# Kernel optimization log

Measured on AMD Instinct MI355X. Metric: run time of the kernel, lower is better.

Reference implementation:

```python
import jax, jax.numpy as jnp
import numpy as np

N = 100000      # nodes
E = 1600000     # edges (avg degree 16)
IN_DIM = 128
OUT_DIM = 64


def setup_inputs() -> dict:
    key = jax.random.key(0)
    k0, k1, k2, k3, k4 = jax.random.split(key, 5)
    h = jax.random.normal(k0, (N, IN_DIM), dtype=jnp.float32)
    src = jax.random.randint(k1, (E,), 0, N)
    dst = jax.random.randint(k2, (E,), 0, N)
    W = jax.random.normal(k3, (OUT_DIM, IN_DIM), dtype=jnp.float32) * 0.05  # fc.weight
    a = jax.random.normal(k4, (2 * OUT_DIM,), dtype=jnp.float32) * 0.05     # attn_fc.weight (flattened)
    return {"h": h, "src": src, "dst": dst, "W": W, "a": a}


def reference(h, src, dst, W, a):
    # z = fc(h)
    z = h @ W.T                                   # [N, OUT_DIM]
    # attn_fc([z_src, z_dst]) == z_src @ a[:D] + z_dst @ a[D:]  (exact linear split)
    s_src = z @ a[:OUT_DIM]                       # [N]
    s_dst = z @ a[OUT_DIM:]                       # [N]
    e = jax.nn.leaky_relu(s_src[src] + s_dst[dst], negative_slope=0.01)  # [E]
    # segment softmax over incoming edges of each dst node
    m = jax.ops.segment_max(e, dst, num_segments=N)
    m = jnp.where(jnp.isfinite(m), m, 0.0)        # empty segments -> -inf; neutralize
    ee = jnp.exp(e - m[dst])                      # [E]
    denom = jax.ops.segment_sum(ee, dst, num_segments=N)
    alpha = ee / jnp.where(denom == 0, 1.0, denom)[dst]
    # scatter-weighted sum of source features
    h_out = jax.ops.segment_sum(alpha[:, None] * z[src], dst, num_segments=N)  # [N, OUT_DIM]
    # activation = F.elu; residual disabled (in_dim != out_dim * num_heads)
    return jax.nn.elu(h_out)
```

## Files before the change

kernel.cpp:

```cpp
#include <hip/hip_runtime.h>
#include <hip/hip_bf16.h>
#include <math.h>

typedef float floatx4 __attribute__((ext_vector_type(4)));
typedef short short8 __attribute__((ext_vector_type(8)));

#define IN_DIM 128
#define OUT_DIM 64
#define OWNER(d) (((d) >> 4) & 7)
#define CHUNK 2048
#define CAP 32
#define OVF_CAP 8192
#define WPAD 136
#define NB_SHIFT 8
#define CELL_CAP 24
#define CHUNK1 4096
#define SPILL_BIT (1 << 20)

__device__ __forceinline__ unsigned short bf16_rne(float f) {
    unsigned u = __float_as_uint(f);
    u += 0x7FFFu + ((u >> 16) & 1u);
    return (unsigned short)(u >> 16);
}
__device__ __forceinline__ float bf16_tof(unsigned short b) {
    return __uint_as_float(((unsigned)b) << 16);
}

__global__ __launch_bounds__(256) void k_gemm(
    const float* __restrict__ h, const float* __restrict__ W,
    const float* __restrict__ a, __hip_bfloat16* __restrict__ z,
    float* __restrict__ s_src, float* __restrict__ s_dst, int N)
{
    __shared__ __align__(16) unsigned short sWhi[64 * WPAD];
    __shared__ __align__(16) unsigned short sWlo[64 * WPAD];

    const int tid = threadIdx.x;
#pragma unroll
    for (int i = 0; i < 32; ++i) {
        int g = tid + 256 * i;
        float f = W[g];
        int row = g >> 7, k = g & 127;
        unsigned short hb = bf16_rne(f);
        sWhi[row * WPAD + k] = hb;
        sWlo[row * WPAD + k] = bf16_rne(f - bf16_tof(hb));
    }

    const int wave = tid >> 6;
    const int l = tid & 63;
    const int lr = l & 15;
    const int lk = l >> 4;
    const int n0w = blockIdx.x * 64 + wave * 16;

    const int arow = min(n0w + lr, N - 1);
    const float* hrow = h + (size_t)arow * IN_DIM;
    short8 ahi[4], alo[4];
#pragma unroll
    for (int ks = 0; ks < 4; ++ks) {
        int k0 = 32 * ks + 8 * lk;
        floatx4 f0 = *(const floatx4*)(hrow + k0);
        floatx4 f1 = *(const floatx4*)(hrow + k0 + 4);
        float fv[8] = {f0.x, f0.y, f0.z, f0.w, f1.x, f1.y, f1.z, f1.w};
#pragma unroll
        for (int j = 0; j < 8; ++j) {
            unsigned short hb = bf16_rne(fv[j]);
            ahi[ks][j] = (short)hb;
            alo[ks][j] = (short)bf16_rne(fv[j] - bf16_tof(hb));
        }
    }
    __syncthreads();

    float ps[4] = {0.f, 0.f, 0.f, 0.f};
    float pd[4] = {0.f, 0.f, 0.f, 0.f};
#pragma unroll
    for (int ct = 0; ct < 4; ++ct) {
        floatx4 acc = (floatx4){0.f, 0.f, 0.f, 0.f};
#pragma unroll
        for (int ks = 0; ks < 4; ++ks) {
            const int boff = (ct * 16 + lr) * WPAD + 32 * ks + 8 * lk;
            short8 bhi = *(const short8*)&sWhi[boff];
            short8 blo = *(const short8*)&sWlo[boff];
            acc = __builtin_amdgcn_mfma_f32_16x16x32_bf16(ahi[ks], bhi, acc, 0, 0, 0);
            acc = __builtin_amdgcn_mfma_f32_16x16x32_bf16(alo[ks], bhi, acc, 0, 0, 0);
            acc = __builtin_amdgcn_mfma_f32_16x16x32_bf16(ahi[ks], blo, acc, 0, 0, 0);
        }
        const float asv = a[ct * 16 + lr];
        const float adv = a[OUT_DIM + ct * 16 + lr];
#pragma unroll
        for (int r = 0; r < 4; ++r) {
            int n = n0w + lk * 4 + r;
            if (n < N)
                z[(size_t)n * OUT_DIM + ct * 16 + lr] = __float2bfloat16(acc[r]);
            ps[r] += acc[r] * asv;
            pd[r] += acc[r] * adv;
        }
    }
#pragma unroll
    for (int r = 0; r < 4; ++r) {
#pragma unroll
        for (int off = 1; off <= 8; off <<= 1) {
            ps[r] += __shfl_xor(ps[r], off);
            pd[r] += __shfl_xor(pd[r], off);
        }
        int n = n0w + lk * 4 + r;
        if (lr == 0 && n < N) {
            s_src[n] = ps[r];
            s_dst[n] = pd[r];
        }
    }
}

__global__ __launch_bounds__(256) void k_bin(
    const int* __restrict__ src, const int* __restrict__ dst,
    int* __restrict__ cursor, unsigned* __restrict__ bdata,
    int* __restrict__ bcnt, int* __restrict__ ovfcnt,
    int2* __restrict__ ovf, int E, int NB)
{
    __shared__ int cell[512];
    const int tid = threadIdx.x;
    for (int i = tid; i < NB; i += 256) cell[i] = 0;
    __syncthreads();

    const int c = blockIdx.x;
    const int e0 = c * CHUNK1;
    const size_t cbase = (size_t)c * NB * CELL_CAP;
#pragma unroll
    for (int i = 0; i < CHUNK1 / 256; ++i) {
        int e = e0 + i * 256 + tid;
        if (e < E) {
            int d = __builtin_nontemporal_load(&dst[e]);
            int s = __builtin_nontemporal_load(&src[e]);
            int b = d >> NB_SHIFT;
            int slot = atomicAdd(&cell[b], 1);
            if (slot < CELL_CAP) {
                bdata[cbase + (size_t)b * CELL_CAP + slot] =
                    ((unsigned)s << 8) | (unsigned)(d & 255);
            } else {
                atomicAdd(&cursor[d], SPILL_BIT);
                int op = atomicAdd(ovfcnt, 1);
                if (op < OVF_CAP) ovf[op] = make_int2(s, d);
            }
        }
    }
    __syncthreads();
    for (int b = tid; b < NB; b += 256) bcnt[c * NB + b] = cell[b];
}

__global__ __launch_bounds__(256) void k_fill(
    const unsigned* __restrict__ bdata, const int* __restrict__ bcnt,
    int* __restrict__ cursor, int* __restrict__ ssort,
    int* __restrict__ ovfcnt, int2* __restrict__ ovf,
    int nb1, int NB, int N)
{
    __shared__ int lcur[256];
    const int tid = threadIdx.x;
    lcur[tid] = 0;
    __syncthreads();

    const int b = blockIdx.x;
    const int n0 = b << NB_SHIFT;
    for (int c = tid; c < nb1; c += 256) {
        int cnt = min(bcnt[c * NB + b], CELL_CAP);
        size_t base = ((size_t)c * NB + b) * CELL_CAP;
        for (int j = 0; j < cnt; ++j) {
            unsigned v = bdata[base + j];
            int i = (int)(v & 255u);
            int s = (int)(v >> 8);
            int slot = atomicAdd(&lcur[i], 1);
            if (slot < CAP) {
                ssort[(n0 + i) * CAP + slot] = s;
            } else {
                int op = atomicAdd(ovfcnt, 1);
                if (op < OVF_CAP) ovf[op] = make_int2(s, n0 + i);
            }
        }
    }
    __syncthreads();
    int n = n0 + tid;
    if (n < N) {
        int v = lcur[tid];
        if (v) cursor[n] += v;
    }
}

__global__ __launch_bounds__(256) void k_scatter(
    const int* __restrict__ src, const int* __restrict__ dst,
    int* __restrict__ cursor, int* __restrict__ ssort,
    int* __restrict__ ovfcnt, int2* __restrict__ ovf, int E)
{
    const int x = blockIdx.x & 7;
    const int c = blockIdx.x >> 3;
    const int e0 = c * CHUNK;
#pragma unroll
    for (int i = 0; i < CHUNK / 256; ++i) {
        int e = e0 + i * 256 + threadIdx.x;
        if (e < E) {
            int d = __builtin_nontemporal_load(&dst[e]);
            if (OWNER(d) == x) {
                int s = __builtin_nontemporal_load(&src[e]);
                int pos = atomicAdd(&cursor[d], 1);
                if (pos < CAP) {
                    ssort[d * CAP + pos] = s;
                } else {
                    int op = atomicAdd(ovfcnt, 1);
                    if (op < OVF_CAP) ovf[op] = make_int2(s, d);
                }
            }
        }
    }
}

__global__ __launch_bounds__(256) void k_node(
    const int* __restrict__ cursor, const int* __restrict__ ssort,
    const float* __restrict__ s_src, const float* __restrict__ s_dst,
    const int* __restrict__ ovfcnt, const int2* __restrict__ ovf,
    const __hip_bfloat16* __restrict__ z, float* __restrict__ out, int N)
{
    const int lane = threadIdx.x & 63;
    const int wave = threadIdx.x >> 6;
    const int n = blockIdx.x * 4 + wave;
    if (n >= N) return;

    const int lg = lane >> 4;
    const int lc = lane & 15;

    const int raw = cursor[n];
    if (raw == 0) {
        if (lg == 0) {
            floatx4 zero = (floatx4){0.f, 0.f, 0.f, 0.f};
            __builtin_nontemporal_store(zero, (floatx4*)&out[(size_t)n * OUT_DIM + 4 * lc]);
        }
        return;
    }
    const int low = raw & 0xFFFFF;
    const int deg = min(low, CAP);
    const int base = n * CAP;
    const float sdn = s_dst[n];

    float sum = 0.f;
    int sv = 0;
    float ev = 0.f;
    {
        int kk = lane;
        if (kk < deg) {
            sv = __builtin_nontemporal_load(&ssort[base + kk]);
            float sc = s_src[sv] + sdn;
            sc = sc > 0.f ? sc : 0.01f * sc;
            ev = __expf(sc);
        }
        sum += ev;
    }

    floatx4 acc = (floatx4){0.f, 0.f, 0.f, 0.f};
    for (int j = 0; j < deg; j += 8) {
        int jj0 = j + lg, jj1 = j + 4 + lg;
        bool ok0 = jj0 < deg, ok1 = jj1 < deg;
        int s0 = __shfl(sv, ok0 ? jj0 : 0);
        int s1 = __shfl(sv, ok1 ? jj1 : 0);
        float w0 = __shfl(ev, ok0 ? jj0 : 0);
        float w1 = __shfl(ev, ok1 ? jj1 : 0);
        w0 = ok0 ? w0 : 0.f;
        w1 = ok1 ? w1 : 0.f;
        int sa0 = ok0 ? s0 : 0;
        int sa1 = ok1 ? s1 : 0;
        uint2 v0 = *(const uint2*)&z[(size_t)sa0 * OUT_DIM + 4 * lc];
        uint2 v1 = *(const uint2*)&z[(size_t)sa1 * OUT_DIM + 4 * lc];
        acc.x += w0 * __uint_as_float(v0.x << 16);
        acc.y += w0 * __uint_as_float(v0.x & 0xFFFF0000u);
        acc.z += w0 * __uint_as_float(v0.y << 16);
        acc.w += w0 * __uint_as_float(v0.y & 0xFFFF0000u);
        acc.x += w1 * __uint_as_float(v1.x << 16);
        acc.y += w1 * __uint_as_float(v1.x & 0xFFFF0000u);
        acc.z += w1 * __uint_as_float(v1.y << 16);
        acc.w += w1 * __uint_as_float(v1.y & 0xFFFF0000u);
    }
    acc.x += __shfl_xor(acc.x, 16); acc.y += __shfl_xor(acc.y, 16);
    acc.z += __shfl_xor(acc.z, 16); acc.w += __shfl_xor(acc.w, 16);
    acc.x += __shfl_xor(acc.x, 32); acc.y += __shfl_xor(acc.y, 32);
    acc.z += __shfl_xor(acc.z, 32); acc.w += __shfl_xor(acc.w, 32);

    if (raw > CAP) {
        int oc = min(*ovfcnt, OVF_CAP);
        for (int i = 0; i < oc; ++i) {
            int2 p = ovf[i];
            if (p.y == n) {
                float sc = s_src[p.x] + sdn;
                sc = sc > 0.f ? sc : 0.01f * sc;
                float e2 = __expf(sc);
                if (lane == 0) sum += e2;
                uint2 v = *(const uint2*)&z[(size_t)p.x * OUT_DIM + 4 * lc];
                acc.x += e2 * __uint_as_float(v.x << 16);
                acc.y += e2 * __uint_as_float(v.x & 0xFFFF0000u);
                acc.z += e2 * __uint_as_float(v.y << 16);
                acc.w += e2 * __uint_as_float(v.y & 0xFFFF0000u);
            }
        }
    }

#pragma unroll
    for (int off = 32; off >= 1; off >>= 1) sum += __shfl_xor(sum, off);

    if (lg == 0) {
        float inv = 1.f / sum;
        floatx4 o;
        o.x = acc.x * inv; o.y = acc.y * inv;
        o.z = acc.z * inv; o.w = acc.w * inv;
        o.x = o.x > 0.f ? o.x : expm1f(o.x);
        o.y = o.y > 0.f ? o.y : expm1f(o.y);
        o.z = o.z > 0.f ? o.z : expm1f(o.z);
        o.w = o.w > 0.f ? o.w : expm1f(o.w);
        __builtin_nontemporal_store(o, (floatx4*)&out[(size_t)n * OUT_DIM + 4 * lc]);
    }
}

extern "C" void kernel_launch(void* const* d_in, const int* in_sizes, int n_in,
                              void* d_out, int out_size, void* d_ws, size_t ws_size,
                              hipStream_t stream)
{
    (void)n_in; (void)out_size;

    const float* h  = (const float*)d_in[0];
    const int* src  = (const int*)d_in[1];
    const int* dst  = (const int*)d_in[2];
    const float* W  = (const float*)d_in[3];
    const float* a  = (const float*)d_in[4];
    const int N = in_sizes[0] / IN_DIM;
    const int E = in_sizes[1];
    float* out = (float*)d_out;

    const int NB  = (N + 255) >> NB_SHIFT;
    const int nb1 = (E + CHUNK1 - 1) / CHUNK1;

    auto rnd = [](size_t b) { return (b + 255) & ~(size_t)255; };
    const size_t meta_ints = (size_t)NB * 256 + 1 + (size_t)nb1 * NB;
    const size_t need_bucket =
        rnd((size_t)N * OUT_DIM * 2) + 2 * rnd((size_t)N * 4) +
        rnd(meta_ints * 4) + rnd((size_t)OVF_CAP * 8) +
        rnd((size_t)N * CAP * 4) + rnd((size_t)nb1 * NB * CELL_CAP * 4);
    const bool bucketed = (NB <= 512) && (need_bucket <= ws_size);

    char* wsp = (char*)d_ws;
    size_t off = 0;
    auto alloc = [&](size_t bytes) -> void* {
        void* p = wsp + off;
        off = (off + bytes + 255) & ~(size_t)255;
        return p;
    };
    __hip_bfloat16* z = (__hip_bfloat16*)alloc((size_t)N * OUT_DIM * 2);
    float* s_src = (float*)alloc((size_t)N * 4);
    float* s_dst = (float*)alloc((size_t)N * 4);

    const int nchunks = (E + CHUNK - 1) / CHUNK;
    k_gemm<<<(N + 63) / 64, 256, 0, stream>>>(h, W, a, z, s_src, s_dst, N);

    if (bucketed) {
        int* cursor = (int*)alloc(meta_ints * 4);
        int* ovfcnt = cursor + (size_t)NB * 256;
        int* bcnt   = ovfcnt + 1;
        int2* ovf   = (int2*)alloc((size_t)OVF_CAP * 8);
        int* ssort  = (int*)alloc((size_t)N * CAP * 4);
        unsigned* bdata = (unsigned*)alloc((size_t)nb1 * NB * CELL_CAP * 4);

        hipMemsetAsync(cursor, 0, meta_ints * 4, stream);
        k_bin<<<nb1, 256, 0, stream>>>(src, dst, cursor, bdata, bcnt,
                                       ovfcnt, ovf, E, NB);
        k_fill<<<NB, 256, 0, stream>>>(bdata, bcnt, cursor, ssort,
                                       ovfcnt, ovf, nb1, NB, N);
        k_node<<<(N + 3) / 4, 256, 0, stream>>>(cursor, ssort, s_src, s_dst,
                                                ovfcnt, ovf, z, out, N);
    } else {
        int* cursor = (int*)alloc((size_t)(N + 1) * 4);
        int* ovfcnt = cursor + N;
        int2* ovf   = (int2*)alloc((size_t)OVF_CAP * 8);
        int* ssort  = (int*)alloc((size_t)N * CAP * 4);

        hipMemsetAsync(cursor, 0, (size_t)(N + 1) * 4, stream);
        k_scatter<<<nchunks * 8, 256, 0, stream>>>(src, dst, cursor, ssort,
                                                   ovfcnt, ovf, E);
        k_node<<<(N + 3) / 4, 256, 0, stream>>>(cursor, ssort, s_src, s_dst,
                                                ovfcnt, ovf, z, out, N);
    }
}
```

Before: 213.6 us.

## Fuse bin and fill kernels with grid barrier, fold memset into GEMM

Merges the binning and fill kernels into one launch that uses a global atomic grid barrier between the two phases. The barrier relies on every block being resident at once (grid of max(NB, nb1) ≈ 391 blocks); if they were not, it would deadlock. The cursor/counter memset is moved into the GEMM kernel, so the separate hipMemsetAsync goes away. The ELU now uses __expf-1 instead of expm1f, which is cheaper but loses accuracy near zero. The aim is to remove launch and memset overhead.

Measured after the change: 267.6 us. 1.25x slower.

```diff
diff --git a/kernel.cpp b/kernel.cpp
--- a/kernel.cpp
+++ b/kernel.cpp
@@ -29,12 +29,16 @@
 __global__ __launch_bounds__(256) void k_gemm(
     const float* __restrict__ h, const float* __restrict__ W,
     const float* __restrict__ a, __hip_bfloat16* __restrict__ z,
-    float* __restrict__ s_src, float* __restrict__ s_dst, int N)
+    float* __restrict__ s_src, float* __restrict__ s_dst, int N,
+    int* __restrict__ meta, int mcount)
 {
     __shared__ __align__(16) unsigned short sWhi[64 * WPAD];
     __shared__ __align__(16) unsigned short sWlo[64 * WPAD];
 
     const int tid = threadIdx.x;
+    for (int i = blockIdx.x * 256 + tid; i < mcount; i += gridDim.x * 256)
+        meta[i] = 0;
+
 #pragma unroll
     for (int i = 0; i < 32; ++i) {
         int g = tid + 256 * i;
@@ -109,62 +113,68 @@
     }
 }
 
-__global__ __launch_bounds__(256) void k_bin(
+__global__ __launch_bounds__(256, 2) void k_binfill(
     const int* __restrict__ src, const int* __restrict__ dst,
     int* __restrict__ cursor, unsigned* __restrict__ bdata,
-    int* __restrict__ bcnt, int* __restrict__ ovfcnt,
-    int2* __restrict__ ovf, int E, int NB)
+    int* __restrict__ bcnt, int* __restrict__ ovfcnt, int* __restrict__ bar,
+    int2* __restrict__ ovf, int* __restrict__ ssort,
+    int E, int NB, int nb1, int N)
 {
     __shared__ int cell[512];
-    const int tid = threadIdx.x;
-    for (int i = tid; i < NB; i += 256) cell[i] = 0;
-    __syncthreads();
-
-    const int c = blockIdx.x;
-    const int e0 = c * CHUNK1;
-    const size_t cbase = (size_t)c * NB * CELL_CAP;
-#pragma unroll
-    for (int i = 0; i < CHUNK1 / 256; ++i) {
-        int e = e0 + i * 256 + tid;
-        if (e < E) {
-            int d = __builtin_nontemporal_load(&dst[e]);
-            int s = __builtin_nontemporal_load(&src[e]);
-            int b = d >> NB_SHIFT;
-            int slot = atomicAdd(&cell[b], 1);
-            if (slot < CELL_CAP) {
-                bdata[cbase + (size_t)b * CELL_CAP + slot] =
-                    ((unsigned)s << 8) | (unsigned)(d & 255);
-            } else {
-                atomicAdd(&cursor[d], SPILL_BIT);
-                int op = atomicAdd(ovfcnt, 1);
-                if (op < OVF_CAP) ovf[op] = make_int2(s, d);
-            }
-        }
-    }
-    __syncthreads();
-    for (int b = tid; b < NB; b += 256) bcnt[c * NB + b] = cell[b];
-}
-
-__global__ __launch_bounds__(256) void k_fill(
-    const unsigned* __restrict__ bdata, const int* __restrict__ bcnt,
-    int* __restrict__ cursor, int* __restrict__ ssort,
-    int* __restrict__ ovfcnt, int2* __restrict__ ovf,
-    int nb1, int NB, int N)
-{
     __shared__ int lcur[256];
     const int tid = threadIdx.x;
+
+    const int c = blockIdx.x;
+    if (c < nb1) {
+        for (int i = tid; i < NB; i += 256) cell[i] = 0;
+        __syncthreads();
+        const int e0 = c * CHUNK1;
+        const size_t cbase = (size_t)c * NB * CELL_CAP;
+#pragma unroll
+        for (int i = 0; i < CHUNK1 / 256; ++i) {
+            int e = e0 + i * 256 + tid;
+            if (e < E) {
+                int d = __builtin_nontemporal_load(&dst[e]);
+                int s = __builtin_nontemporal_load(&src[e]);
+                int b = d >> NB_SHIFT;
+                int slot = atomicAdd(&cell[b], 1);
+                if (slot < CELL_CAP) {
+                    bdata[cbase + (size_t)b * CELL_CAP + slot] =
+                        ((unsigned)s << NB_SHIFT) |
+                        (unsigned)(d & ((1 << NB_SHIFT) - 1));
+                } else {
+                    atomicAdd(&cursor[d], SPILL_BIT);
+                    int op = atomicAdd(ovfcnt, 1);
+                    if (op < OVF_CAP) ovf[op] = make_int2(s, d);
+                }
+            }
+        }
+        __syncthreads();
+        for (int b = tid; b < NB; b += 256) bcnt[c * NB + b] = cell[b];
+    }
+
+    __syncthreads();
+    if (tid == 0) {
+        __hip_atomic_fetch_add(bar, 1, __ATOMIC_RELEASE, __HIP_MEMORY_SCOPE_AGENT);
+        while (__hip_atomic_load(bar, __ATOMIC_ACQUIRE, __HIP_MEMORY_SCOPE_AGENT)
+               < (int)gridDim.x)
+            __builtin_amdgcn_s_sleep(8);
+    }
+    __syncthreads();
+
+    const int b = blockIdx.x;
+    if (b >= NB) return;
     lcur[tid] = 0;
     __syncthreads();
 
-    const int b = blockIdx.x;
     const int n0 = b << NB_SHIFT;
-    for (int c = tid; c < nb1; c += 256) {
-        int cnt = min(bcnt[c * NB + b], CELL_CAP);
-        size_t base = ((size_t)c * NB + b) * CELL_CAP;
+    for (int cc = tid; cc < nb1; cc += 256) {
+        int cnt = min(bcnt[cc * NB + b], CELL_CAP);
+        size_t base = ((size_t)cc * NB + b) * CELL_CAP;
         for (int j = 0; j < cnt; ++j) {
             unsigned v = bdata[base + j];
-            int i = (int)(v & 255u);
-            int s = (int)(v >> 8);
+            int i = (int)(v & ((1u << NB_SHIFT) - 1));
+            int s = (int)(v >> NB_SHIFT);
             int slot = atomicAdd(&lcur[i], 1);
             if (slot < CAP) {
                 ssort[(n0 + i) * CAP + slot] = s;
@@ -176,7 +186,7 @@
     }
     __syncthreads();
     int n = n0 + tid;
-    if (n < N) {
+    if (tid < (1 << NB_SHIFT) && n < N) {
         int v = lcur[tid];
         if (v) cursor[n] += v;
     }
@@ -304,10 +314,10 @@
         floatx4 o;
         o.x = acc.x * inv; o.y = acc.y * inv;
         o.z = acc.z * inv; o.w = acc.w * inv;
-        o.x = o.x > 0.f ? o.x : expm1f(o.x);
-        o.y = o.y > 0.f ? o.y : expm1f(o.y);
-        o.z = o.z > 0.f ? o.z : expm1f(o.z);
-        o.w = o.w > 0.f ? o.w : expm1f(o.w);
+        o.x = o.x > 0.f ? o.x : __expf(o.x) - 1.f;
+        o.y = o.y > 0.f ? o.y : __expf(o.y) - 1.f;
+        o.z = o.z > 0.f ? o.z : __expf(o.z) - 1.f;
+        o.w = o.w > 0.f ? o.w : __expf(o.w) - 1.f;
         __builtin_nontemporal_store(o, (floatx4*)&out[(size_t)n * OUT_DIM + 4 * lc]);
     }
 }
@@ -327,16 +337,17 @@
     const int E = in_sizes[1];
     float* out = (float*)d_out;
 
-    const int NB  = (N + 255) >> NB_SHIFT;
+    const int NB  = (N + (1 << NB_SHIFT) - 1) >> NB_SHIFT;
     const int nb1 = (E + CHUNK1 - 1) / CHUNK1;
+    const int g   = NB > nb1 ? NB : nb1;
 
     auto rnd = [](size_t b) { return (b + 255) & ~(size_t)255; };
-    const size_t meta_ints = (size_t)NB * 256 + 1 + (size_t)nb1 * NB;
+    const size_t meta_ints = (size_t)N + 2 + (size_t)nb1 * NB;
     const size_t need_bucket =
         rnd((size_t)N * OUT_DIM * 2) + 2 * rnd((size_t)N * 4) +
         rnd(meta_ints * 4) + rnd((size_t)OVF_CAP * 8) +
         rnd((size_t)N * CAP * 4) + rnd((size_t)nb1 * NB * CELL_CAP * 4);
-    const bool bucketed = (NB <= 512) && (need_bucket <= ws_size);
+    const bool bucketed = (NB <= 512) && (g <= 512) && (need_bucket <= ws_size);
 
     char* wsp = (char*)d_ws;
     size_t off = 0;
@@ -349,31 +360,31 @@
     float* s_src = (float*)alloc((size_t)N * 4);
     float* s_dst = (float*)alloc((size_t)N * 4);
 
-    const int nchunks = (E + CHUNK - 1) / CHUNK;
-    k_gemm<<<(N + 63) / 64, 256, 0, stream>>>(h, W, a, z, s_src, s_dst, N);
-
     if (bucketed) {
         int* cursor = (int*)alloc(meta_ints * 4);
-        int* ovfcnt = cursor + (size_t)NB * 256;
-        int* bcnt   = ovfcnt + 1;
+        int* ovfcnt = cursor + N;
+        int* bar    = cursor + N + 1;
+        int* bcnt   = cursor + N + 2;
         int2* ovf   = (int2*)alloc((size_t)OVF_CAP * 8);
         int* ssort  = (int*)alloc((size_t)N * CAP * 4);
         unsigned* bdata = (unsigned*)alloc((size_t)nb1 * NB * CELL_CAP * 4);
 
-        hipMemsetAsync(cursor, 0, meta_ints * 4, stream);
-        k_bin<<<nb1, 256, 0, stream>>>(src, dst, cursor, bdata, bcnt,
-                                       ovfcnt, ovf, E, NB);
-        k_fill<<<NB, 256, 0, stream>>>(bdata, bcnt, cursor, ssort,
-                                       ovfcnt, ovf, nb1, NB, N);
+        k_gemm<<<(N + 63) / 64, 256, 0, stream>>>(h, W, a, z, s_src, s_dst, N,
+                                                  cursor, N + 2);
+        k_binfill<<<g, 256, 0, stream>>>(src, dst, cursor, bdata, bcnt,
+                                         ovfcnt, bar, ovf, ssort,
+                                         E, NB, nb1, N);
         k_node<<<(N + 3) / 4, 256, 0, stream>>>(cursor, ssort, s_src, s_dst,
                                                 ovfcnt, ovf, z, out, N);
     } else {
-        int* cursor = (int*)alloc((size_t)(N + 1) * 4);
+        int* cursor = (int*)alloc((size_t)(N + 2) * 4);
         int* ovfcnt = cursor + N;
         int2* ovf   = (int2*)alloc((size_t)OVF_CAP * 8);
         int* ssort  = (int*)alloc((size_t)N * CAP * 4);
 
-        hipMemsetAsync(cursor, 0, (size_t)(N + 1) * 4, stream);
+        const int nchunks = (E + CHUNK - 1) / CHUNK;
+        k_gemm<<<(N + 63) / 64, 256, 0, stream>>>(h, W, a, z, s_src, s_dst, N,
+                                                  cursor, N + 2);
         k_scatter<<<nchunks * 8, 256, 0, stream>>>(src, dst, cursor, ssort,
                                                    ovfcnt, ovf, E);
         k_node<<<(N + 3) / 4, 256, 0, stream>>>(cursor, ssort, s_src, s_dst,
```
